# Kernel optimization log

Measured on AMD Instinct MI355X. Metric: run time of the kernel, lower is better.

Reference implementation:

```python
import jax, jax.numpy as jnp
import numpy as np
from jax import lax

HIDDEN = 256
WIDTH = 1024
DEPTH = 4
T = 64
SUBSTEPS = 8  # fixed RK4 substeps per save interval (replaces diffrax adaptive Tsit5)

Y0 = np.array([0.0008417, 0.01495894, 0.00082556, 0.00068982, 0.00063456,
               0.00832867, 0.00190631, 0.00155624, 0.00142264, 0.01858621,
               0.02000239, 0.01796071, 0.01670121, 0.22218046, 0.02531468,
               0.03337227, 0.6147068], dtype=np.float32)


def setup_inputs() -> dict:
    key = jax.random.key(0)
    ks = jax.random.split(key, 8)

    def lin(k, out, inp):
        kw, kb = jax.random.split(k)
        lim = 1.0 / np.sqrt(inp)
        W = jax.random.uniform(kw, (out, inp), jnp.float32, -lim, lim)
        b = jax.random.uniform(kb, (out,), jnp.float32, -lim, lim)
        return W, b

    W0, b0 = lin(ks[0], WIDTH, HIDDEN + 17)
    Whs, bhs = [], []
    for i in range(DEPTH - 1):
        w, b = lin(ks[1 + i], WIDTH, WIDTH)
        Whs.append(w)
        bhs.append(b)
    Wh = jnp.stack(Whs)   # [DEPTH-1, WIDTH, WIDTH]
    bh = jnp.stack(bhs)   # [DEPTH-1, WIDTH]
    Wl, bl = lin(ks[4], HIDDEN, WIDTH)
    beta_W, beta_b = lin(ks[5], 1, HIDDEN)
    hvec = 0.01 * jax.random.normal(ks[6], (HIDDEN,), jnp.float32)
    scale = jnp.array([0.1], jnp.float32)
    y0_log = jnp.log(jnp.asarray(Y0))
    ts = jnp.arange(T, dtype=jnp.float32) * 0.25  # save points (months)
    return dict(ts=ts, W0=W0, b0=b0, Wh=Wh, bh=bh, Wl=Wl, bl=bl,
                beta_W=beta_W, beta_b=beta_b, hvec=hvec, scale=scale,
                y0_log=y0_log)


def _forward(ts, W0, b0, Wh, bh, Wl, bl, beta_W, beta_b, hvec, scale, y0_log):
    xi, mu, sigma, nu, gamma = 13/12, 0.041/12, 91/12, 36/12, 1.8/12

    def mlp(x):  # softplus hidden activations, final tanh(0.01*x)
        z = jax.nn.softplus(W0 @ x + b0)
        def body(z, wb):
            w, b = wb
            return jax.nn.softplus(w @ z + b), None
        z, _ = lax.scan(body, z, (Wh, bh))
        return jnp.tanh(0.01 * (Wl @ z + bl))

    def rhs(y):  # y = concat(state[17], h[HIDDEN])
        state, h = y[:17], y[17:]
        bb1 = 8.0 * jax.nn.sigmoid(beta_W @ h + beta_b)[0] + 25.0
        bb2, bb3, bb4 = 0.5 * bb1, 0.35 * bb1, 0.25 * bb1
        M, S1, E1, E2, E3, E4, I1, I2, I3, I4, R1, R2, R3, R4, S2, S3, S4 = state
        I = I1 + I2 + I3 + I4
        R = R1 + R2 + R3 + R4
        dstate = jnp.stack([
            R * mu - (xi + mu) * M,
            mu * (1 - R) + xi * M - mu * S1 - bb1 * I * S1,
            bb1 * I * S1 - (mu + sigma) * E1,
            bb2 * I * S2 - (mu + sigma) * E2,
            bb3 * I * S3 - (mu + sigma) * E3,
            bb4 * I * S4 - (mu + sigma) * E4,
            sigma * E1 - (nu + mu) * I1,
            sigma * E2 - (nu + mu) * I2,
            sigma * E3 - (nu + mu) * I3,
            sigma * E4 - (nu + mu) * I4,
            nu * I1 - (mu + gamma) * R1,
            nu * I2 - (mu + gamma) * R2,
            nu * I3 - (mu + gamma) * R3,
            nu * I4 - (mu + gamma) * R4,
            gamma * R1 - mu * S2 - bb2 * I * S2,
            gamma * R2 - mu * S3 - bb3 * I * S3,
            gamma * (R3 + R4) - mu * S4 - bb4 * I * S4,
        ])
        dh = scale[0] * mlp(jnp.concatenate([h, state]))
        return jnp.concatenate([dstate, dh])

    def rk4(y, dt):
        k1 = rhs(y)
        k2 = rhs(y + 0.5 * dt * k1)
        k3 = rhs(y + 0.5 * dt * k2)
        k4 = rhs(y + dt * k3)
        return y + (dt / 6.0) * (k1 + 2 * k2 + 2 * k3 + k4)

    y0 = jnp.concatenate([jax.nn.softmax(y0_log), hvec])

    def interval(y, dt_i):
        dt = dt_i / SUBSTEPS
        def step(y, _):
            return rk4(y, dt), None
        y, _ = lax.scan(step, y, None, length=SUBSTEPS)
        return y, y

    dts = ts[1:] - ts[:-1]
    _, ys = lax.scan(interval, y0, dts)
    ys = jnp.concatenate([y0[None], ys], axis=0)  # [T, 17+HIDDEN]
    return ys[:, :17], ys[:, 17:]


def reference(ts, W0, b0, Wh, bh, Wl, bl, beta_W, beta_b, hvec, scale, y0_log):
    return _forward(ts, W0, b0, Wh, bh, Wl, bl, beta_W, beta_b, hvec, scale, y0_log)
```

## Files before the change

### kernel.cpp

```cpp
#include <hip/hip_runtime.h>
#include <math.h>

#define NBLK    32
#define NLAUNCH 256
#define BS      512
#define NSTATE  17
#define NH      256
#define NX      273
#define WID     1024
#define NT      64
#define NSUB    8
#define ROWS_H  (WID/NBLK)
#define ROWS_L  (NH/NBLK)
#define POLL_CAP 2000000

typedef unsigned long long u64;

__device__ __forceinline__ float softplus_f(float v) {
    return fmaxf(v, 0.f) + log1pf(expf(-fabsf(v)));
}

__device__ __forceinline__ void st_l2(u64* p, float v, unsigned tag) {
    unsigned lo = __float_as_uint(v);
    u64 w = ((u64)(tag ^ lo) << 32) | (u64)lo;
    asm volatile("global_atomic_swap_x2 %0, %1, off" :: "v"(p), "v"(w) : "memory");
}
__device__ __forceinline__ u64 ld_l2(const u64* p) {
    u64 w;
    asm volatile("global_atomic_add_x2 %0, %1, %2, off sc0\n\t"
                 "s_waitcnt vmcnt(0)"
                 : "=&v"(w) : "v"(p), "v"(0ULL) : "memory");
    return w;
}
__device__ __forceinline__ void ld_l2_pair(const u64* p0, const u64* p1,
                                           u64& w0, u64& w1) {
    asm volatile("global_atomic_add_x2 %0, %2, %4, off sc0\n\t"
                 "global_atomic_add_x2 %1, %3, %4, off sc0\n\t"
                 "s_waitcnt vmcnt(0)"
                 : "=&v"(w0), "=&v"(w1) : "v"(p0), "v"(p1), "v"(0ULL) : "memory");
}
__device__ __forceinline__ bool tag_ok(u64 w, unsigned tag) {
    return ((unsigned)(w >> 32) ^ (unsigned)w) == tag;
}

__device__ __forceinline__ void poll_z(const u64* __restrict__ buf, unsigned tag,
                                       float* __restrict__ z_s, int t,
                                       volatile int* dead) {
    const u64* p0 = buf + t;
    const u64* p1 = buf + t + 512;
    u64 w0 = 0, w1 = 0;
    int it = 0;
    for (;;) {
        ld_l2_pair(p0, p1, w0, w1);
        if (tag_ok(w0, tag) & tag_ok(w1, tag)) break;
        if (++it > POLL_CAP) *dead = 1;
        if (*dead) break;
    }
    z_s[t]       = __uint_as_float((unsigned)w0);
    z_s[t + 512] = __uint_as_float((unsigned)w1);
    __syncthreads();
}

extern "C" __global__ __launch_bounds__(BS, 2) void ode_kernel(
    const float* __restrict__ ts,   const float* __restrict__ W0,
    const float* __restrict__ b0,   const float* __restrict__ Wh,
    const float* __restrict__ bh,   const float* __restrict__ Wl,
    const float* __restrict__ bl,   const float* __restrict__ betaW,
    const float* __restrict__ betab,const float* __restrict__ hvec,
    const float* __restrict__ scale,const float* __restrict__ y0log,
    float* __restrict__ out, u64* zA, u64* zB, u64* dhb, unsigned* ctrl)
{
    const int t = threadIdx.x;

    __shared__ int      role_sh;
    __shared__ unsigned tagbase_sh;
    __shared__ int      dead_sh;
    __shared__ float y_s[NX];
    __shared__ float yn_s[NX];
    __shared__ float xm[NX];
    __shared__ float k_s[NX];
    __shared__ float z_s[WID];
    __shared__ float red[8];
    __shared__ float dt_sh;
    extern __shared__ float wh2[];

    if (t == 0) {
        int xcd;
        asm volatile("s_getreg_b32 %0, hwreg(HW_REG_XCC_ID)" : "=s"(xcd));
        xcd &= 7;
        unsigned rk = atomicAdd(&ctrl[xcd], 1u);
        if (rk == NBLK - 1) {
            u64 rt;
            asm volatile("s_memrealtime %0\n\ts_waitcnt lgkmcnt(0)" : "=s"(rt));
            unsigned word = (((unsigned)(rt >> 4)) << 4) | (unsigned)(xcd + 1);
            atomicCAS(&ctrl[8], 0u, word);
        }
        unsigned w; int it = 0;
        do {
            w = __hip_atomic_load(&ctrl[8], __ATOMIC_RELAXED, __HIP_MEMORY_SCOPE_AGENT);
        } while (w == 0u && ++it < POLL_CAP);
        int winner = (int)(w & 0xFu) - 1;
        role_sh    = (w != 0u && xcd == winner && rk < NBLK) ? (int)rk : -1;
        tagbase_sh = w;
        dead_sh    = 0;
    }
    __syncthreads();
    const int blk = role_sh;
    const unsigned tagbase = tagbase_sh;
    if (blk < 0) return;

    const float scale0 = scale[0];
    const float betab0 = betab[0];
    unsigned R = 0;

    const int rowH = t >> 4, laneH = t & 15;
    const int growH = blk * ROWS_H + rowH;
    const int rowL = t >> 6, laneL = t & 63;
    const int growL = blk * ROWS_L + rowL;

    const float b0r = b0[growH];
    float bhr[3];
    bhr[0] = bh[growH]; bhr[1] = bh[WID + growH]; bhr[2] = bh[2 * WID + growH];
    const float blr    = bl[growL];
    const float betaWr = (t < NH) ? betaW[t] : 0.f;
    const float* wlp = Wl + (size_t)growL * WID + laneL * 4;

    float4 wv0[16], wv1[16];
    {
        const float* whp = Wh + (size_t)growH * WID + laneH * 4;
        #pragma unroll
        for (int i = 0; i < 16; i++) wv0[i] = *(const float4*)(whp + i * 64);
        #pragma unroll
        for (int i = 0; i < 16; i++) wv1[i] = *(const float4*)(whp + WID * WID + i * 64);
    }
    {
        const float* src = Wh + 2 * (size_t)WID * WID + (size_t)blk * ROWS_H * WID;
        for (int i = t * 4; i < ROWS_H * WID; i += BS * 4)
            *(float4*)&wh2[i] = *(const float4*)&src[i];
    }
    float w0r[18];
    {
        const float* w0p = W0 + (size_t)growH * NX;
        #pragma unroll
        for (int i = 0; i < 18; i++) {
            int c = laneH + i * 16;
            w0r[i] = (c < NX) ? w0p[c] : 0.f;
        }
    }

    if (t < NSTATE) {
        float m = -1e30f;
        for (int j = 0; j < NSTATE; j++) m = fmaxf(m, y0log[j]);
        float ssum = 0.f;
        for (int j = 0; j < NSTATE; j++) ssum += expf(y0log[j] - m);
        y_s[t] = expf(y0log[t] - m) / ssum;
    }
    if (t < NH) y_s[NSTATE + t] = hvec[t];
    __syncthreads();

    if (blk == 0) {
        if (t < NSTATE) out[t] = y_s[t];
        if (t < NH)     out[NT * NSTATE + t] = y_s[NSTATE + t];
    }

    const float c_xi = 13.f / 12.f, c_mu = 0.041f / 12.f, c_sig = 91.f / 12.f,
                c_nu = 36.f / 12.f, c_gam = 1.8f / 12.f;

    for (int iv = 0; iv < NT - 1; iv++) {
        if (t == 0) dt_sh = (ts[iv + 1] - ts[iv]) * (1.f / NSUB);
        __syncthreads();
        const float dt = dt_sh;

        for (int sub = 0; sub < NSUB; sub++) {
            if (t < NX) yn_s[t] = y_s[t];

            for (int s = 0; s < 4; s++) {
                const float a   = (s == 0) ? 0.f : ((s == 3) ? 1.f : 0.5f);
                const float wgt = ((s == 0) || (s == 3)) ? dt * (1.f / 6.f) : dt * (1.f / 3.f);
                const float adt = a * dt;

                if (t < NX) {
                    const int src = (t < NH) ? (NSTATE + t) : (t - NH);
                    float v = y_s[src];
                    if (s != 0) v = fmaf(adt, k_s[src], v);
                    xm[t] = v;
                }
                __syncthreads();

                {
                    float acc = 0.f;
                    #pragma unroll
                    for (int i = 0; i < 18; i++) {
                        int c = laneH + i * 16;
                        if (c < NX) acc = fmaf(w0r[i], xm[c], acc);
                    }
                    #pragma unroll
                    for (int m = 1; m < 16; m <<= 1) acc += __shfl_xor(acc, m, 16);
                    ++R;
                    if (laneH == 0) st_l2(&zA[growH], softplus_f(acc + b0r), tagbase + R);
                }

                {
                    if (t < NH) {
                        float p = betaWr * xm[t];
                        #pragma unroll
                        for (int m = 1; m < 64; m <<= 1) p += __shfl_xor(p, m, 64);
                        if ((t & 63) == 0) red[t >> 6] = p;
                    }
                    __syncthreads();
                    if (t == 0) {
                        const float* xs = xm + NH;
                        float sd  = red[0] + red[1] + red[2] + red[3] + betab0;
                        float bb1 = 8.f / (1.f + expf(-sd)) + 25.f;
                        float bb2 = 0.5f * bb1, bb3 = 0.35f * bb1, bb4 = 0.25f * bb1;
                        float M  = xs[0],  S1 = xs[1],  E1 = xs[2],  E2 = xs[3];
                        float E3 = xs[4],  E4 = xs[5],  I1 = xs[6],  I2 = xs[7];
                        float I3 = xs[8],  I4 = xs[9],  R1 = xs[10], R2 = xs[11];
                        float R3 = xs[12], R4 = xs[13], S2 = xs[14], S3 = xs[15];
                        float S4 = xs[16];
                        float I = I1 + I2 + I3 + I4, Rs = R1 + R2 + R3 + R4;
                        k_s[0]  = Rs * c_mu - (c_xi + c_mu) * M;
                        k_s[1]  = c_mu * (1.f - Rs) + c_xi * M - c_mu * S1 - bb1 * I * S1;
                        k_s[2]  = bb1 * I * S1 - (c_mu + c_sig) * E1;
                        k_s[3]  = bb2 * I * S2 - (c_mu + c_sig) * E2;
                        k_s[4]  = bb3 * I * S3 - (c_mu + c_sig) * E3;
                        k_s[5]  = bb4 * I * S4 - (c_mu + c_sig) * E4;
                        k_s[6]  = c_sig * E1 - (c_nu + c_mu) * I1;
                        k_s[7]  = c_sig * E2 - (c_nu + c_mu) * I2;
                        k_s[8]  = c_sig * E3 - (c_nu + c_mu) * I3;
                        k_s[9]  = c_sig * E4 - (c_nu + c_mu) * I4;
                        k_s[10] = c_nu * I1 - (c_mu + c_gam) * R1;
                        k_s[11] = c_nu * I2 - (c_mu + c_gam) * R2;
                        k_s[12] = c_nu * I3 - (c_mu + c_gam) * R3;
                        k_s[13] = c_nu * I4 - (c_mu + c_gam) * R4;
                        k_s[14] = c_gam * R1 - c_mu * S2 - bb2 * I * S2;
                        k_s[15] = c_gam * R2 - c_mu * S3 - bb3 * I * S3;
                        k_s[16] = c_gam * (R3 + R4) - c_mu * S4 - bb4 * I * S4;
                    }
                }

                auto hidden = [&](const float4 (&wv)[16], const u64* zin,
                                  u64* zout, float bias) {
                    poll_z(zin, tagbase + R, z_s, t, &dead_sh);
                    float acc = 0.f;
                    #pragma unroll
                    for (int i = 0; i < 16; i++) {
                        float4 zv = *(const float4*)(z_s + (laneH * 4 + i * 64));
                        acc = fmaf(wv[i].x, zv.x, acc);
                        acc = fmaf(wv[i].y, zv.y, acc);
                        acc = fmaf(wv[i].z, zv.z, acc);
                        acc = fmaf(wv[i].w, zv.w, acc);
                    }
                    #pragma unroll
                    for (int m = 1; m < 16; m <<= 1) acc += __shfl_xor(acc, m, 16);
                    ++R;
                    if (laneH == 0) st_l2(&zout[growH], softplus_f(acc + bias), tagbase + R);
                };

                hidden(wv0, zA, zB, bhr[0]);
                hidden(wv1, zB, zA, bhr[1]);

                float4 wvL[4];
                #pragma unroll
                for (int i = 0; i < 4; i++) wvL[i] = *(const float4*)(wlp + i * 256);

                {
                    poll_z(zA, tagbase + R, z_s, t, &dead_sh);
                    const float* wr = wh2 + rowH * WID + laneH * 4;
                    float acc = 0.f;
                    #pragma unroll
                    for (int i = 0; i < 16; i++) {
                        float4 wv4 = *(const float4*)(wr + i * 64);
                        float4 zv  = *(const float4*)(z_s + (laneH * 4 + i * 64));
                        acc = fmaf(wv4.x, zv.x, acc);
                        acc = fmaf(wv4.y, zv.y, acc);
                        acc = fmaf(wv4.z, zv.z, acc);
                        acc = fmaf(wv4.w, zv.w, acc);
                    }
                    #pragma unroll
                    for (int m = 1; m < 16; m <<= 1) acc += __shfl_xor(acc, m, 16);
                    ++R;
                    if (laneH == 0) st_l2(&zB[growH], softplus_f(acc + bhr[2]), tagbase + R);
                }

                {
                    poll_z(zB, tagbase + R, z_s, t, &dead_sh);
                    float acc = 0.f;
                    #pragma unroll
                    for (int i = 0; i < 4; i++) {
                        float4 zv = *(const float4*)(z_s + (laneL * 4 + i * 256));
                        acc = fmaf(wvL[i].x, zv.x, acc);
                        acc = fmaf(wvL[i].y, zv.y, acc);
                        acc = fmaf(wvL[i].z, zv.z, acc);
                        acc = fmaf(wvL[i].w, zv.w, acc);
                    }
                    #pragma unroll
                    for (int m = 1; m < 64; m <<= 1) acc += __shfl_xor(acc, m, 64);
                    ++R;
                    if (laneL == 0)
                        st_l2(&dhb[growL], scale0 * tanhf(0.01f * (acc + blr)), tagbase + R);
                }

                {
                    if (t < NH) {
                        u64 w; int it = 0;
                        volatile int* dead = &dead_sh;
                        for (;;) {
                            w = ld_l2(dhb + t);
                            if (tag_ok(w, tagbase + R)) break;
                            if (++it > POLL_CAP) *dead = 1;
                            if (*dead) break;
                        }
                        k_s[NSTATE + t] = __uint_as_float((unsigned)w);
                    }
                    __syncthreads();
                    if (t < NX) yn_s[t] = fmaf(wgt, k_s[t], yn_s[t]);
                }
            }

            __syncthreads();
            if (t < NX) y_s[t] = yn_s[t];
            __syncthreads();
        }

        if (blk == 0) {
            if (t < NSTATE) out[(iv + 1) * NSTATE + t] = y_s[t];
            if (t < NH)     out[NT * NSTATE + (iv + 1) * NH + t] = y_s[NSTATE + t];
        }
    }
}

extern "C" void kernel_launch(void* const* d_in, const int* in_sizes, int n_in,
                              void* d_out, int out_size, void* d_ws, size_t ws_size,
                              hipStream_t stream) {
    const float* ts    = (const float*)d_in[0];
    const float* W0    = (const float*)d_in[1];
    const float* b0    = (const float*)d_in[2];
    const float* Wh    = (const float*)d_in[3];
    const float* bh    = (const float*)d_in[4];
    const float* Wl    = (const float*)d_in[5];
    const float* bl    = (const float*)d_in[6];
    const float* betaW = (const float*)d_in[7];
    const float* betab = (const float*)d_in[8];
    const float* hvec  = (const float*)d_in[9];
    const float* scale = (const float*)d_in[10];
    const float* y0log = (const float*)d_in[11];
    float* out = (float*)d_out;

    u64*      zA   = (u64*)d_ws;
    u64*      zB   = (u64*)((char*)d_ws + 8192);
    u64*      dhb  = (u64*)((char*)d_ws + 16384);
    unsigned* ctrl = (unsigned*)((char*)d_ws + 18432);

    static int lds_set = 0;
    if (!lds_set) {
        hipFuncSetAttribute((const void*)ode_kernel,
                            hipFuncAttributeMaxDynamicSharedMemorySize, 131072);
        lds_set = 1;
    }

    hipMemsetAsync(d_ws, 0, 18432 + 64, stream);
    hipLaunchKernelGGL(ode_kernel, dim3(NLAUNCH), dim3(BS), 131072, stream,
                       ts, W0, b0, Wh, bh, Wl, bl, betaW, betab, hvec, scale,
                       y0log, out, zA, zB, dhb, ctrl);
}
```

Before: 25.21 ms.

## Replace per-element tagged atomic polling with block-counter flags and plain stores

```diff
diff --git a/kernel.cpp b/kernel.cpp
--- a/kernel.cpp
+++ b/kernel.cpp
@@ -14,50 +14,46 @@
 #define ROWS_L  (NH/NBLK)
 #define POLL_CAP 2000000
 
-typedef unsigned long long u64;
+typedef unsigned int u32;
 
 __device__ __forceinline__ float softplus_f(float v) {
     return fmaxf(v, 0.f) + log1pf(expf(-fabsf(v)));
 }
 
-__device__ __forceinline__ void st_l2(u64* p, float v, unsigned tag) {
-    unsigned lo = __float_as_uint(v);
-    u64 w = ((u64)(tag ^ lo) << 32) | (u64)lo;
-    asm volatile("global_atomic_swap_x2 %0, %1, off" :: "v"(p), "v"(w) : "memory");
-}
-__device__ __forceinline__ u64 ld_l2(const u64* p) {
-    u64 w;
-    asm volatile("global_atomic_add_x2 %0, %1, %2, off sc0\n\t"
+#define FLG_STRIDE 16
+
+__device__ __forceinline__ void flag_add(u32* flags, unsigned R) {
+    u32* fp = flags + (R & 7) * FLG_STRIDE;
+    asm volatile("global_atomic_add %0, %1, off" :: "v"(fp), "v"(1u) : "memory");
+}
+__device__ __forceinline__ u32 flag_read(u32* flags, unsigned R) {
+    u32* fp = flags + (R & 7) * FLG_STRIDE;
+    u32 cur;
+    asm volatile("global_atomic_add %0, %1, %2, off sc0\n\t"
                  "s_waitcnt vmcnt(0)"
-                 : "=&v"(w) : "v"(p), "v"(0ULL) : "memory");
-    return w;
-}
-__device__ __forceinline__ void ld_l2_pair(const u64* p0, const u64* p1,
-                                           u64& w0, u64& w1) {
-    asm volatile("global_atomic_add_x2 %0, %2, %4, off sc0\n\t"
-                 "global_atomic_add_x2 %1, %3, %4, off sc0\n\t"
-                 "s_waitcnt vmcnt(0)"
-                 : "=&v"(w0), "=&v"(w1) : "v"(p0), "v"(p1), "v"(0ULL) : "memory");
-}
-__device__ __forceinline__ bool tag_ok(u64 w, unsigned tag) {
-    return ((unsigned)(w >> 32) ^ (unsigned)w) == tag;
-}
-
-__device__ __forceinline__ void poll_z(const u64* __restrict__ buf, unsigned tag,
-                                       float* __restrict__ z_s, int t,
-                                       volatile int* dead) {
-    const u64* p0 = buf + t;
-    const u64* p1 = buf + t + 512;
-    u64 w0 = 0, w1 = 0;
-    int it = 0;
-    for (;;) {
-        ld_l2_pair(p0, p1, w0, w1);
-        if (tag_ok(w0, tag) & tag_ok(w1, tag)) break;
-        if (++it > POLL_CAP) *dead = 1;
-        if (*dead) break;
-    }
-    z_s[t]       = __uint_as_float((unsigned)w0);
-    z_s[t + 512] = __uint_as_float((unsigned)w1);
+                 : "=&v"(cur) : "v"(fp), "v"(0u) : "memory");
+    return cur;
+}
+__device__ __forceinline__ void publish(u32* flags, unsigned R, int t) {
+    asm volatile("s_waitcnt vmcnt(0)" ::: "memory");
+    __syncthreads();
+    if (t == 0) flag_add(flags, R);
+}
+__device__ __forceinline__ void wait_flag(u32* flags, unsigned R, int t) {
+    if (t == 0) {
+        const unsigned tgt = (unsigned)NBLK * (((R - 1) >> 3) + 1);
+        int it = 0;
+        while (flag_read(flags, R) < tgt && ++it < POLL_CAP) {}
+    }
+    __syncthreads();
+    asm volatile("buffer_inv" ::: "memory");
+}
+__device__ __forceinline__ void consume_z(const float* __restrict__ buf,
+                                          u32* flags, unsigned R,
+                                          float* __restrict__ z_s, int t) {
+    wait_flag(flags, R, t);
+    float2 v = *(const float2*)(buf + 2 * t);
+    *(float2*)(z_s + 2 * t) = v;
     __syncthreads();
 }
 
@@ -68,13 +64,12 @@
     const float* __restrict__ bl,   const float* __restrict__ betaW,
     const float* __restrict__ betab,const float* __restrict__ hvec,
     const float* __restrict__ scale,const float* __restrict__ y0log,
-    float* __restrict__ out, u64* zA, u64* zB, u64* dhb, unsigned* ctrl)
+    float* __restrict__ out, float* zA, float* zB, float* dhb,
+    u32* flags, unsigned* ctrl)
 {
     const int t = threadIdx.x;
 
-    __shared__ int      role_sh;
-    __shared__ unsigned tagbase_sh;
-    __shared__ int      dead_sh;
+    __shared__ int   role_sh;
     __shared__ float y_s[NX];
     __shared__ float yn_s[NX];
     __shared__ float xm[NX];
@@ -89,24 +84,15 @@
         asm volatile("s_getreg_b32 %0, hwreg(HW_REG_XCC_ID)" : "=s"(xcd));
         xcd &= 7;
         unsigned rk = atomicAdd(&ctrl[xcd], 1u);
-        if (rk == NBLK - 1) {
-            u64 rt;
-            asm volatile("s_memrealtime %0\n\ts_waitcnt lgkmcnt(0)" : "=s"(rt));
-            unsigned word = (((unsigned)(rt >> 4)) << 4) | (unsigned)(xcd + 1);
-            atomicCAS(&ctrl[8], 0u, word);
-        }
+        if (rk == NBLK - 1) atomicCAS(&ctrl[8], 0u, (unsigned)(xcd + 1));
         unsigned w; int it = 0;
         do {
             w = __hip_atomic_load(&ctrl[8], __ATOMIC_RELAXED, __HIP_MEMORY_SCOPE_AGENT);
         } while (w == 0u && ++it < POLL_CAP);
-        int winner = (int)(w & 0xFu) - 1;
-        role_sh    = (w != 0u && xcd == winner && rk < NBLK) ? (int)rk : -1;
-        tagbase_sh = w;
-        dead_sh    = 0;
+        role_sh = (w != 0u && xcd == (int)w - 1 && rk < NBLK) ? (int)rk : -1;
     }
     __syncthreads();
     const int blk = role_sh;
-    const unsigned tagbase = tagbase_sh;
     if (blk < 0) return;
 
     const float scale0 = scale[0];
@@ -196,8 +182,9 @@
                     }
                     #pragma unroll
                     for (int m = 1; m < 16; m <<= 1) acc += __shfl_xor(acc, m, 16);
+                    if (laneH == 0) zA[growH] = softplus_f(acc + b0r);
                     ++R;
-                    if (laneH == 0) st_l2(&zA[growH], softplus_f(acc + b0r), tagbase + R);
+                    publish(flags, R, t);
                 }
 
                 {
@@ -239,9 +226,9 @@
                     }
                 }
 
-                auto hidden = [&](const float4 (&wv)[16], const u64* zin,
-                                  u64* zout, float bias) {
-                    poll_z(zin, tagbase + R, z_s, t, &dead_sh);
+                auto hidden = [&](const float4 (&wv)[16], const float* zin,
+                                  float* zout, float bias) {
+                    consume_z(zin, flags, R, z_s, t);
                     float acc = 0.f;
                     #pragma unroll
                     for (int i = 0; i < 16; i++) {
@@ -253,8 +240,9 @@
                     }
                     #pragma unroll
                     for (int m = 1; m < 16; m <<= 1) acc += __shfl_xor(acc, m, 16);
+                    if (laneH == 0) zout[growH] = softplus_f(acc + bias);
                     ++R;
-                    if (laneH == 0) st_l2(&zout[growH], softplus_f(acc + bias), tagbase + R);
+                    publish(flags, R, t);
                 };
 
                 hidden(wv0, zA, zB, bhr[0]);
@@ -265,7 +253,7 @@
                 for (int i = 0; i < 4; i++) wvL[i] = *(const float4*)(wlp + i * 256);
 
                 {
-                    poll_z(zA, tagbase + R, z_s, t, &dead_sh);
+                    consume_z(zA, flags, R, z_s, t);
                     const float* wr = wh2 + rowH * WID + laneH * 4;
                     float acc = 0.f;
                     #pragma unroll
@@ -279,12 +267,13 @@
                     }
                     #pragma unroll
                     for (int m = 1; m < 16; m <<= 1) acc += __shfl_xor(acc, m, 16);
+                    if (laneH == 0) zB[growH] = softplus_f(acc + bhr[2]);
                     ++R;
-                    if (laneH == 0) st_l2(&zB[growH], softplus_f(acc + bhr[2]), tagbase + R);
-                }
-
-                {
-                    poll_z(zB, tagbase + R, z_s, t, &dead_sh);
+                    publish(flags, R, t);
+                }
+
+                {
+                    consume_z(zB, flags, R, z_s, t);
                     float acc = 0.f;
                     #pragma unroll
                     for (int i = 0; i < 4; i++) {
@@ -296,23 +285,14 @@
                     }
                     #pragma unroll
                     for (int m = 1; m < 64; m <<= 1) acc += __shfl_xor(acc, m, 64);
+                    if (laneL == 0) dhb[growL] = scale0 * tanhf(0.01f * (acc + blr));
                     ++R;
-                    if (laneL == 0)
-                        st_l2(&dhb[growL], scale0 * tanhf(0.01f * (acc + blr)), tagbase + R);
-                }
-
-                {
-                    if (t < NH) {
-                        u64 w; int it = 0;
-                        volatile int* dead = &dead_sh;
-                        for (;;) {
-                            w = ld_l2(dhb + t);
-                            if (tag_ok(w, tagbase + R)) break;
-                            if (++it > POLL_CAP) *dead = 1;
-                            if (*dead) break;
-                        }
-                        k_s[NSTATE + t] = __uint_as_float((unsigned)w);
-                    }
+                    publish(flags, R, t);
+                }
+
+                {
+                    wait_flag(flags, R, t);
+                    if (t < NH) k_s[NSTATE + t] = dhb[t];
                     __syncthreads();
                     if (t < NX) yn_s[t] = fmaf(wgt, k_s[t], yn_s[t]);
                 }
@@ -347,10 +327,11 @@
     const float* y0log = (const float*)d_in[11];
     float* out = (float*)d_out;
 
-    u64*      zA   = (u64*)d_ws;
-    u64*      zB   = (u64*)((char*)d_ws + 8192);
-    u64*      dhb  = (u64*)((char*)d_ws + 16384);
-    unsigned* ctrl = (unsigned*)((char*)d_ws + 18432);
+    float*    zA    = (float*)d_ws;
+    float*    zB    = (float*)((char*)d_ws + 4096);
+    float*    dhb   = (float*)((char*)d_ws + 8192);
+    u32*      flags = (u32*)((char*)d_ws + 9216);
+    unsigned* ctrl  = (unsigned*)((char*)d_ws + 9728);
 
     static int lds_set = 0;
     if (!lds_set) {
@@ -359,8 +340,8 @@
         lds_set = 1;
     }
 
-    hipMemsetAsync(d_ws, 0, 18432 + 64, stream);
+    hipMemsetAsync(d_ws, 0, 10240, stream);
     hipLaunchKernelGGL(ode_kernel, dim3(NLAUNCH), dim3(BS), 131072, stream,
                        ts, W0, b0, Wh, bh, Wl, bl, betaW, betab, hvec, scale,
-                       y0log, out, zA, zB, dhb, ctrl);
-}
+                       y0log, out, zA, zB, dhb, flags, ctrl);
+}
```

Result: faster. 22.30 ms (-11.5%).

## Use 16 blocks of 1024 threads and stream hidden weights from global memory

Applied to the files above, without the earlier changes.

```diff
diff --git a/kernel.cpp b/kernel.cpp
--- a/kernel.cpp
+++ b/kernel.cpp
@@ -1,9 +1,9 @@
 #include <hip/hip_runtime.h>
 #include <math.h>
 
-#define NBLK    32
+#define NBLK    16
 #define NLAUNCH 256
-#define BS      512
+#define BS      1024
 #define NSTATE  17
 #define NH      256
 #define NX      273
@@ -15,74 +15,59 @@
 #define POLL_CAP 2000000
 
 typedef unsigned long long u64;
+typedef unsigned int u32;
 
 __device__ __forceinline__ float softplus_f(float v) {
     return fmaxf(v, 0.f) + log1pf(expf(-fabsf(v)));
 }
 
-__device__ __forceinline__ void st_l2(u64* p, float v, unsigned tag) {
+__device__ __forceinline__ void st_tag(u64* p, float v, unsigned tag) {
     unsigned lo = __float_as_uint(v);
     u64 w = ((u64)(tag ^ lo) << 32) | (u64)lo;
     asm volatile("global_atomic_swap_x2 %0, %1, off" :: "v"(p), "v"(w) : "memory");
 }
-__device__ __forceinline__ u64 ld_l2(const u64* p) {
+__device__ __forceinline__ u64 ld_tag(const u64* p) {
     u64 w;
     asm volatile("global_atomic_add_x2 %0, %1, %2, off sc0\n\t"
                  "s_waitcnt vmcnt(0)"
                  : "=&v"(w) : "v"(p), "v"(0ULL) : "memory");
     return w;
 }
-__device__ __forceinline__ void ld_l2_pair(const u64* p0, const u64* p1,
-                                           u64& w0, u64& w1) {
-    asm volatile("global_atomic_add_x2 %0, %2, %4, off sc0\n\t"
-                 "global_atomic_add_x2 %1, %3, %4, off sc0\n\t"
-                 "s_waitcnt vmcnt(0)"
-                 : "=&v"(w0), "=&v"(w1) : "v"(p0), "v"(p1), "v"(0ULL) : "memory");
-}
 __device__ __forceinline__ bool tag_ok(u64 w, unsigned tag) {
-    return ((unsigned)(w >> 32) ^ (unsigned)w) == tag;
-}
-
-__device__ __forceinline__ void poll_z(const u64* __restrict__ buf, unsigned tag,
-                                       float* __restrict__ z_s, int t,
-                                       volatile int* dead) {
-    const u64* p0 = buf + t;
-    const u64* p1 = buf + t + 512;
-    u64 w0 = 0, w1 = 0;
-    int it = 0;
-    for (;;) {
-        ld_l2_pair(p0, p1, w0, w1);
-        if (tag_ok(w0, tag) & tag_ok(w1, tag)) break;
-        if (++it > POLL_CAP) *dead = 1;
-        if (*dead) break;
-    }
-    z_s[t]       = __uint_as_float((unsigned)w0);
-    z_s[t + 512] = __uint_as_float((unsigned)w1);
+    return (((u32)(w >> 32)) ^ ((u32)w)) == tag;
+}
+
+__device__ __forceinline__ void consume_z(const u64* __restrict__ buf,
+                                          unsigned tag,
+                                          float* __restrict__ z_s, int t) {
     __syncthreads();
-}
-
-extern "C" __global__ __launch_bounds__(BS, 2) void ode_kernel(
+    const u64* p = buf + t;
+    u64 w; int it = 0;
+    do { w = ld_tag(p); } while (!tag_ok(w, tag) && ++it < POLL_CAP);
+    z_s[t] = __uint_as_float((u32)w);
+    __syncthreads();
+}
+
+extern "C" __global__ __launch_bounds__(BS, 4) void ode_kernel(
     const float* __restrict__ ts,   const float* __restrict__ W0,
     const float* __restrict__ b0,   const float* __restrict__ Wh,
     const float* __restrict__ bh,   const float* __restrict__ Wl,
     const float* __restrict__ bl,   const float* __restrict__ betaW,
     const float* __restrict__ betab,const float* __restrict__ hvec,
     const float* __restrict__ scale,const float* __restrict__ y0log,
-    float* __restrict__ out, u64* zA, u64* zB, u64* dhb, unsigned* ctrl)
+    float* __restrict__ out, u64* zA64, u64* zB64, u64* dh64, unsigned* ctrl)
 {
     const int t = threadIdx.x;
 
     __shared__ int      role_sh;
     __shared__ unsigned tagbase_sh;
-    __shared__ int      dead_sh;
     __shared__ float y_s[NX];
     __shared__ float yn_s[NX];
     __shared__ float xm[NX];
     __shared__ float k_s[NX];
     __shared__ float z_s[WID];
-    __shared__ float red[8];
+    __shared__ float red[4];
     __shared__ float dt_sh;
-    extern __shared__ float wh2[];
 
     if (t == 0) {
         int xcd;
@@ -99,10 +84,8 @@
         do {
             w = __hip_atomic_load(&ctrl[8], __ATOMIC_RELAXED, __HIP_MEMORY_SCOPE_AGENT);
         } while (w == 0u && ++it < POLL_CAP);
-        int winner = (int)(w & 0xFu) - 1;
-        role_sh    = (w != 0u && xcd == winner && rk < NBLK) ? (int)rk : -1;
+        role_sh    = (w != 0u && xcd == (int)(w & 0xFu) - 1 && rk < NBLK) ? (int)rk : -1;
         tagbase_sh = w;
-        dead_sh    = 0;
     }
     __syncthreads();
     const int blk = role_sh;
@@ -123,21 +106,11 @@
     bhr[0] = bh[growH]; bhr[1] = bh[WID + growH]; bhr[2] = bh[2 * WID + growH];
     const float blr    = bl[growL];
     const float betaWr = (t < NH) ? betaW[t] : 0.f;
-    const float* wlp = Wl + (size_t)growL * WID + laneL * 4;
-
-    float4 wv0[16], wv1[16];
-    {
-        const float* whp = Wh + (size_t)growH * WID + laneH * 4;
-        #pragma unroll
-        for (int i = 0; i < 16; i++) wv0[i] = *(const float4*)(whp + i * 64);
-        #pragma unroll
-        for (int i = 0; i < 16; i++) wv1[i] = *(const float4*)(whp + WID * WID + i * 64);
-    }
-    {
-        const float* src = Wh + 2 * (size_t)WID * WID + (size_t)blk * ROWS_H * WID;
-        for (int i = t * 4; i < ROWS_H * WID; i += BS * 4)
-            *(float4*)&wh2[i] = *(const float4*)&src[i];
-    }
+    const float* wh0p = Wh + (size_t)growH * WID + laneH * 4;
+    const float* wh1p = wh0p + (size_t)WID * WID;
+    const float* wh2p = wh1p + (size_t)WID * WID;
+    const float* wlp  = Wl + (size_t)growL * WID + laneL * 4;
+
     float w0r[18];
     {
         const float* w0p = W0 + (size_t)growH * NX;
@@ -197,7 +170,7 @@
                     #pragma unroll
                     for (int m = 1; m < 16; m <<= 1) acc += __shfl_xor(acc, m, 16);
                     ++R;
-                    if (laneH == 0) st_l2(&zA[growH], softplus_f(acc + b0r), tagbase + R);
+                    if (laneH == 0) st_tag(&zA64[growH], softplus_f(acc + b0r), tagbase + R);
                 }
 
                 {
@@ -239,9 +212,14 @@
                     }
                 }
 
-                auto hidden = [&](const float4 (&wv)[16], const u64* zin,
-                                  u64* zout, float bias) {
-                    poll_z(zin, tagbase + R, z_s, t, &dead_sh);
+                auto hidden = [&](const float* wp, const u64* zin64,
+                                  u64* zout64, float bias) {
+                    float4 wv[16];
+                    #pragma unroll
+                    for (int i = 0; i < 16; i++) wv[i] = *(const float4*)(wp + i * 64);
+
+                    consume_z(zin64, tagbase + R, z_s, t);
+
                     float acc = 0.f;
                     #pragma unroll
                     for (int i = 0; i < 16; i++) {
@@ -254,37 +232,20 @@
                     #pragma unroll
                     for (int m = 1; m < 16; m <<= 1) acc += __shfl_xor(acc, m, 16);
                     ++R;
-                    if (laneH == 0) st_l2(&zout[growH], softplus_f(acc + bias), tagbase + R);
+                    if (laneH == 0) st_tag(&zout64[growH], softplus_f(acc + bias), tagbase + R);
                 };
 
-                hidden(wv0, zA, zB, bhr[0]);
-                hidden(wv1, zB, zA, bhr[1]);
-
-                float4 wvL[4];
-                #pragma unroll
-                for (int i = 0; i < 4; i++) wvL[i] = *(const float4*)(wlp + i * 256);
+                hidden(wh0p, zA64, zB64, bhr[0]);
+                hidden(wh1p, zB64, zA64, bhr[1]);
+                hidden(wh2p, zA64, zB64, bhr[2]);
 
                 {
-                    poll_z(zA, tagbase + R, z_s, t, &dead_sh);
-                    const float* wr = wh2 + rowH * WID + laneH * 4;
-                    float acc = 0.f;
-                    #pragma unroll
-                    for (int i = 0; i < 16; i++) {
-                        float4 wv4 = *(const float4*)(wr + i * 64);
-                        float4 zv  = *(const float4*)(z_s + (laneH * 4 + i * 64));
-                        acc = fmaf(wv4.x, zv.x, acc);
-                        acc = fmaf(wv4.y, zv.y, acc);
-                        acc = fmaf(wv4.z, zv.z, acc);
-                        acc = fmaf(wv4.w, zv.w, acc);
-                    }
-                    #pragma unroll
-                    for (int m = 1; m < 16; m <<= 1) acc += __shfl_xor(acc, m, 16);
-                    ++R;
-                    if (laneH == 0) st_l2(&zB[growH], softplus_f(acc + bhr[2]), tagbase + R);
-                }
-
-                {
-                    poll_z(zB, tagbase + R, z_s, t, &dead_sh);
+                    float4 wvL[4];
+                    #pragma unroll
+                    for (int i = 0; i < 4; i++) wvL[i] = *(const float4*)(wlp + i * 256);
+
+                    consume_z(zB64, tagbase + R, z_s, t);
+
                     float acc = 0.f;
                     #pragma unroll
                     for (int i = 0; i < 4; i++) {
@@ -298,20 +259,15 @@
                     for (int m = 1; m < 64; m <<= 1) acc += __shfl_xor(acc, m, 64);
                     ++R;
                     if (laneL == 0)
-                        st_l2(&dhb[growL], scale0 * tanhf(0.01f * (acc + blr)), tagbase + R);
+                        st_tag(&dh64[growL], scale0 * tanhf(0.01f * (acc + blr)), tagbase + R);
                 }
 
                 {
                     if (t < NH) {
                         u64 w; int it = 0;
-                        volatile int* dead = &dead_sh;
-                        for (;;) {
-                            w = ld_l2(dhb + t);
-                            if (tag_ok(w, tagbase + R)) break;
-                            if (++it > POLL_CAP) *dead = 1;
-                            if (*dead) break;
-                        }
-                        k_s[NSTATE + t] = __uint_as_float((unsigned)w);
+                        do { w = ld_tag(dh64 + t); }
+                        while (!tag_ok(w, tagbase + R) && ++it < POLL_CAP);
+                        k_s[NSTATE + t] = __uint_as_float((u32)w);
                     }
                     __syncthreads();
                     if (t < NX) yn_s[t] = fmaf(wgt, k_s[t], yn_s[t]);
@@ -347,20 +303,13 @@
     const float* y0log = (const float*)d_in[11];
     float* out = (float*)d_out;
 
-    u64*      zA   = (u64*)d_ws;
-    u64*      zB   = (u64*)((char*)d_ws + 8192);
-    u64*      dhb  = (u64*)((char*)d_ws + 16384);
+    u64*      zA64 = (u64*)d_ws;
+    u64*      zB64 = (u64*)((char*)d_ws + 8192);
+    u64*      dh64 = (u64*)((char*)d_ws + 16384);
     unsigned* ctrl = (unsigned*)((char*)d_ws + 18432);
 
-    static int lds_set = 0;
-    if (!lds_set) {
-        hipFuncSetAttribute((const void*)ode_kernel,
-                            hipFuncAttributeMaxDynamicSharedMemorySize, 131072);
-        lds_set = 1;
-    }
-
     hipMemsetAsync(d_ws, 0, 18432 + 64, stream);
-    hipLaunchKernelGGL(ode_kernel, dim3(NLAUNCH), dim3(BS), 131072, stream,
+    hipLaunchKernelGGL(ode_kernel, dim3(NLAUNCH), dim3(BS), 0, stream,
                        ts, W0, b0, Wh, bh, Wl, bl, betaW, betab, hvec, scale,
-                       y0log, out, zA, zB, dhb, ctrl);
-}
+                       y0log, out, zA64, zB64, dh64, ctrl);
+}
```

Measured after the change: 56.14 ms. 123% more time.
